# Optimization experiments

Hardware: AMD Instinct MI355X
Metric: run time of the kernel (lower is better)

The kernel has to match this reference:

```python
import jax, jax.numpy as jnp
import numpy as np

B, S, IN_DIM, HID, OUT_DIM, H = 2, 2048, 1024, 1024, 1024, 16
DH_IN = IN_DIM // H   # 64
DH_HID = HID // H     # 64


def setup_inputs() -> dict:
    key = jax.random.key(0)
    ks = jax.random.split(key, 12)
    sc_in = 1.0 / np.sqrt(DH_IN)
    sc_hid = 1.0 / np.sqrt(HID)
    return {
        "q": jax.random.normal(ks[0], (B, S, IN_DIM), jnp.float32),
        "k": jax.random.normal(ks[1], (B, S, IN_DIM), jnp.float32),
        "v": jax.random.normal(ks[2], (B, S, IN_DIM), jnp.float32),
        "mask": jax.random.randint(ks[3], (B, 1, S, S), 0, 2, jnp.int32),
        "Wq": jax.random.uniform(ks[4], (DH_HID, DH_IN), jnp.float32, -sc_in, sc_in),
        "bq": jax.random.uniform(ks[5], (DH_HID,), jnp.float32, -sc_in, sc_in),
        "Wk": jax.random.uniform(ks[6], (DH_HID, DH_IN), jnp.float32, -sc_in, sc_in),
        "bk": jax.random.uniform(ks[7], (DH_HID,), jnp.float32, -sc_in, sc_in),
        "Wv": jax.random.uniform(ks[8], (DH_HID, DH_IN), jnp.float32, -sc_in, sc_in),
        "bv": jax.random.uniform(ks[9], (DH_HID,), jnp.float32, -sc_in, sc_in),
        "Wo": jax.random.uniform(ks[10], (OUT_DIM, HID), jnp.float32, -sc_hid, sc_hid),
        "bo": jax.random.uniform(ks[11], (OUT_DIM,), jnp.float32, -sc_hid, sc_hid),
    }


def reference(q, k, v, mask, Wq, bq, Wk, bk, Wv, bv, Wo, bo):
    # Faithful to original: raw reshape head split (view), NOT a transpose split.
    q_i = q.reshape(B, H, S, DH_IN) @ Wq.T + bq   # [B,H,S,DH_HID]
    k_i = k.reshape(B, H, S, DH_IN) @ Wk.T + bk
    v_i = v.reshape(B, H, S, DH_IN) @ Wv.T + bv
    scores = jnp.einsum('bhqd,bhkd->bhqk', q_i, k_i) / jnp.sqrt(jnp.float32(DH_HID))
    scores = jnp.where(mask != 0, jnp.float32(-10000.0), scores)
    wv = jnp.einsum('bhqk,bhkd->bhqd', jax.nn.softmax(scores, axis=-1), v_i)
    # Faithful to original: raw reshape merge [B,H,S,dh] -> [B,S,H*dh].
    wv = wv.reshape(B, S, H * DH_HID)
    return wv @ Wo.T + bo
```

## Files before the change

### kernel.cpp

```cpp
#include <hip/hip_runtime.h>
#include <hip/hip_bf16.h>
#include <hip/hip_fp16.h>

#define NB 2
#define NS 2048
#define NHD 16
#define DH 64
#define NHID 1024
#define SD (NS*DH)
#define BHN (NB*NHD)

typedef _Float16 F16;
typedef _Float16 f16x8 __attribute__((ext_vector_type(8)));
typedef _Float16 f16x2 __attribute__((ext_vector_type(2)));
typedef float    f32x4  __attribute__((ext_vector_type(4)));
typedef float    f32x16 __attribute__((ext_vector_type(16)));
typedef unsigned short U16;
typedef unsigned long long U64;
typedef unsigned short u16x8 __attribute__((ext_vector_type(8)));

__device__ __forceinline__ f32x4 mfma16(f16x8 a, f16x8 b, f32x4 c) {
  return __builtin_amdgcn_mfma_f32_16x16x32_f16(a, b, c, 0, 0, 0);
}
__device__ __forceinline__ f32x16 mfma32(f16x8 a, f16x8 b, f32x16 c) {
  return __builtin_amdgcn_mfma_f32_32x32x16_f16(a, b, c, 0, 0, 0);
}
__device__ __forceinline__ unsigned pk2(float a, float b) {
  return __builtin_bit_cast(unsigned, __builtin_amdgcn_cvt_pkrtz(a, b));
}

__global__ __launch_bounds__(256) void k_prep(const int* __restrict__ mask,
                                              const float* __restrict__ Wo,
                                              U64* __restrict__ mb,
                                              F16* __restrict__ wob) {
  const int tid  = threadIdx.x;
  const int lane = tid & 63;
  const int wid  = blockIdx.x * 4 + (tid >> 6);
  const int nwords = NB * NS * (NS / 64);
  for (int w = wid; w < nwords; w += 4096) {
    int m = mask[(size_t)w * 64 + lane];
    U64 bits = __ballot(m != 0);
    if (lane == 0) mb[w] = bits;
  }
  int t = blockIdx.x * 256 + tid;
  float4 f = *(const float4*)(Wo + (size_t)t * 4);
  union { U16 u[4]; F16 h[4]; } o;
  o.h[0] = (F16)f.x; o.h[1] = (F16)f.y; o.h[2] = (F16)f.z; o.h[3] = (F16)f.w;
  *(ushort4*)(wob + (size_t)t * 4) = *(ushort4*)o.u;
}

__global__ __launch_bounds__(256) void k_proj(const float* __restrict__ qin,
    const float* __restrict__ kin, const float* __restrict__ vin,
    const float* __restrict__ Wq, const float* __restrict__ bq,
    const float* __restrict__ Wk, const float* __restrict__ bk,
    const float* __restrict__ Wv, const float* __restrict__ bv,
    F16* __restrict__ qh, F16* __restrict__ kh, F16* __restrict__ vt) {
  __shared__ float Xs[64][68];
  __shared__ F16   Ws[64][72];
  __shared__ float bs[64];
  __shared__ F16   Ts[64][72];

  const int tid = threadIdx.x;
  const int bh = blockIdx.x >> 5;
  const int rt = blockIdx.x & 31;
  const int b = bh >> 4, h = bh & 15;
  const int r0 = rt * 64;
  const size_t xbase = (size_t)b * NS * NHID + (size_t)h * SD + (size_t)r0 * DH;
  const int w = tid >> 6, lane = tid & 63, lm = lane & 15, lg = lane >> 4;
  (void)h;

  for (int t = 0; t < 3; ++t) {
    const float* Xin = (t == 0) ? qin : (t == 1) ? kin : vin;
    const float* Wt  = (t == 0) ? Wq  : (t == 1) ? Wk  : Wv;
    const float* bt  = (t == 0) ? bq  : (t == 1) ? bk  : bv;
    const float scale = (t == 0) ? 0.18033688f : 1.0f;
    __syncthreads();
#pragma unroll
    for (int it = 0; it < 4; ++it) {
      int f = it * 1024 + tid * 4;
      int r = f >> 6, c = f & 63;
      float4 xv = *(const float4*)(Xin + xbase + f);
      *(float4*)&Xs[r][c] = xv;
      float4 wv4 = *(const float4*)(Wt + f);
      union { U16 u[4]; F16 h4[4]; } wo;
      wo.h4[0] = (F16)(wv4.x * scale); wo.h4[1] = (F16)(wv4.y * scale);
      wo.h4[2] = (F16)(wv4.z * scale); wo.h4[3] = (F16)(wv4.w * scale);
      *(ushort4*)&Ws[r][c] = *(ushort4*)wo.u;
    }
    if (tid < 64) bs[tid] = bt[tid] * scale;
    __syncthreads();

    f16x8 af[2];
#pragma unroll
    for (int kk = 0; kk < 2; ++kk) {
      const float* sp = &Xs[w * 16 + lm][kk * 32 + lg * 8];
      union { F16 h8[8]; f16x8 v; } pk;
#pragma unroll
      for (int j = 0; j < 8; ++j) pk.h8[j] = (F16)sp[j];
      af[kk] = pk.v;
    }
    f32x4 acc[4];
#pragma unroll
    for (int nt = 0; nt < 4; ++nt) acc[nt] = (f32x4){0.f, 0.f, 0.f, 0.f};
#pragma unroll
    for (int kk = 0; kk < 2; ++kk) {
#pragma unroll
      for (int nt = 0; nt < 4; ++nt) {
        f16x8 bw = *(const f16x8*)&Ws[nt * 16 + lm][kk * 32 + lg * 8];
        acc[nt] = mfma16(af[kk], bw, acc[nt]);
      }
    }
    if (t < 2) {
      F16* dst = (t == 0) ? qh : kh;
#pragma unroll
      for (int nt = 0; nt < 4; ++nt)
#pragma unroll
        for (int rg = 0; rg < 4; ++rg) {
          int row = w * 16 + lg * 4 + rg;
          int col = nt * 16 + lm;
          dst[(size_t)bh * SD + (size_t)(r0 + row) * DH + col] =
              (F16)(acc[nt][rg] + bs[col]);
        }
    } else {
#pragma unroll
      for (int nt = 0; nt < 4; ++nt)
#pragma unroll
        for (int rg = 0; rg < 4; ++rg) {
          int row = w * 16 + lg * 4 + rg;
          int col = nt * 16 + lm;
          Ts[row][col] = (F16)(acc[nt][rg] + bs[col]);
        }
      __syncthreads();
      int d = tid >> 2, qq = tid & 3;
      size_t dst = (size_t)bh * SD + (size_t)d * NS + r0 + qq * 16;
#pragma unroll
      for (int half = 0; half < 2; ++half) {
        union { F16 h8[8]; u16x8 v; } pk;
#pragma unroll
        for (int i = 0; i < 8; ++i) {
          int r = (i < 4) ? (half * 4 + i) : (i + 4 + half * 4);
          pk.h8[i] = Ts[qq * 16 + r][d];
        }
        *(u16x8*)(vt + dst + half * 8) = pk.v;
      }
    }
  }
}

__global__ __launch_bounds__(256) void k_attn(const F16* __restrict__ qh,
    const F16* __restrict__ kh, const F16* __restrict__ vt,
    const U64* __restrict__ mb, F16* __restrict__ wvb) {
  __shared__ float bl[4][32];
  const int tid = threadIdx.x;
  const int w = tid >> 6, l = tid & 63;
  const int lq = l & 31, hi = l >> 5;
  const int tile = blockIdx.x * 4 + w;
  const int bh = tile >> 6;
  const int qt = tile & 63;
  const int b = bh >> 4;
  const int q0 = qt * 32;
  const size_t hb = (size_t)bh * SD;

  f16x8 qf[4];
#pragma unroll
  for (int kt = 0; kt < 4; ++kt)
    qf[kt] = *(const f16x8*)(qh + hb + (size_t)(q0 + lq) * DH + kt * 16 + hi * 8);

  f32x16 accO0, accO1;
#pragma unroll
  for (int r = 0; r < 16; ++r) { accO0[r] = 0.f; accO1[r] = 0.f; }
  float m_run = -1e30f, l_run = 0.f;

  const U64* mrow = mb + ((size_t)b * NS + q0 + lq) * (NS / 64);
  const F16* kb = kh + hb;
  const F16* vb = vt + hb;
  const f16x2 one2 = {(F16)1.f, (F16)1.f};

  for (int c64 = 0; c64 < 32; ++c64) {
    const int kv0 = c64 * 64;
    U64 wm = mrow[c64];
    f32x16 s0, s1;
#pragma unroll
    for (int r = 0; r < 16; ++r) { s0[r] = 0.f; s1[r] = 0.f; }
#pragma unroll
    for (int kt = 0; kt < 4; ++kt) {
      f16x8 kf0 = *(const f16x8*)(kb + (size_t)(kv0 + lq) * DH + kt * 16 + hi * 8);
      f16x8 kf1 = *(const f16x8*)(kb + (size_t)(kv0 + 32 + lq) * DH + kt * 16 + hi * 8);
      s0 = mfma32(kf0, qf[kt], s0);
      s1 = mfma32(kf1, qf[kt], s1);
    }
    float cmax = fmaxf(s0[0], s1[0]);
#pragma unroll
    for (int r = 1; r < 16; ++r) cmax = fmaxf(cmax, fmaxf(s0[r], s1[r]));
    cmax = fmaxf(cmax, __shfl_xor(cmax, 32, 64));
    if (__any(cmax > m_run + 8.0f)) {
      float nm = fmaxf(m_run, cmax);
      float al = __builtin_amdgcn_exp2f(m_run - nm);
      m_run = nm;
      l_run *= al;
      bl[w][lq] = al;
      asm volatile("s_waitcnt lgkmcnt(0)" ::: "memory");
      __builtin_amdgcn_sched_barrier(0);
      float4 g0 = *(const float4*)&bl[w][hi * 4];
      float4 g1 = *(const float4*)&bl[w][8 + hi * 4];
      float4 g2 = *(const float4*)&bl[w][16 + hi * 4];
      float4 g3 = *(const float4*)&bl[w][24 + hi * 4];
      float av[16] = {g0.x,g0.y,g0.z,g0.w, g1.x,g1.y,g1.z,g1.w,
                      g2.x,g2.y,g2.z,g2.w, g3.x,g3.y,g3.z,g3.w};
#pragma unroll
      for (int r = 0; r < 16; ++r) { accO0[r] *= av[r]; accO1[r] *= av[r]; }
    }
#pragma unroll
    for (int r = 0; r < 16; ++r) {
      s0[r] = __builtin_amdgcn_exp2f(s0[r] - m_run);
      s1[r] = __builtin_amdgcn_exp2f(s1[r] - m_run);
    }
    unsigned u0 = ((unsigned)wm) >> (hi * 4);
    unsigned u1 = ((unsigned)(wm >> 32)) >> (hi * 4);
#pragma unroll
    for (int r = 0; r < 16; ++r) {
      const int sh = (r & 3) + 8 * (r >> 2);
      s0[r] = ((u0 >> sh) & 1u) ? 0.f : s0[r];
      s1[r] = ((u1 >> sh) & 1u) ? 0.f : s1[r];
    }
#pragma unroll
    for (int c = 0; c < 4; ++c) {
      const int rb = (c & 1) * 8;
      unsigned w0, w1, w2, w3;
      if (c < 2) {
        w0 = pk2(s0[rb + 0], s0[rb + 1]);
        w1 = pk2(s0[rb + 2], s0[rb + 3]);
        w2 = pk2(s0[rb + 4], s0[rb + 5]);
        w3 = pk2(s0[rb + 6], s0[rb + 7]);
      } else {
        w0 = pk2(s1[rb + 0], s1[rb + 1]);
        w1 = pk2(s1[rb + 2], s1[rb + 3]);
        w2 = pk2(s1[rb + 4], s1[rb + 5]);
        w3 = pk2(s1[rb + 6], s1[rb + 7]);
      }
      union { unsigned u[4]; f16x8 v; } P;
      P.u[0] = w0; P.u[1] = w1; P.u[2] = w2; P.u[3] = w3;
      l_run = __builtin_amdgcn_fdot2(__builtin_bit_cast(f16x2, w0), one2, l_run, false);
      l_run = __builtin_amdgcn_fdot2(__builtin_bit_cast(f16x2, w1), one2, l_run, false);
      l_run = __builtin_amdgcn_fdot2(__builtin_bit_cast(f16x2, w2), one2, l_run, false);
      l_run = __builtin_amdgcn_fdot2(__builtin_bit_cast(f16x2, w3), one2, l_run, false);
      f16x8 v0 = *(const f16x8*)(vb + (size_t)lq * NS + kv0 + c * 16 + hi * 8);
      f16x8 v1 = *(const f16x8*)(vb + (size_t)(32 + lq) * NS + kv0 + c * 16 + hi * 8);
      accO0 = mfma32(P.v, v0, accO0);
      accO1 = mfma32(P.v, v1, accO1);
    }
  }
  l_run += __shfl_xor(l_run, 32, 64);
  float inv = 1.0f / l_run;
  bl[w][lq] = inv;
  asm volatile("s_waitcnt lgkmcnt(0)" ::: "memory");
  __builtin_amdgcn_sched_barrier(0);
  float4 g0 = *(const float4*)&bl[w][hi * 4];
  float4 g1 = *(const float4*)&bl[w][8 + hi * 4];
  float4 g2 = *(const float4*)&bl[w][16 + hi * 4];
  float4 g3 = *(const float4*)&bl[w][24 + hi * 4];
  float iv[16] = {g0.x,g0.y,g0.z,g0.w, g1.x,g1.y,g1.z,g1.w,
                  g2.x,g2.y,g2.z,g2.w, g3.x,g3.y,g3.z,g3.w};
#pragma unroll
  for (int r = 0; r < 16; ++r) {
    const int row = q0 + (r & 3) + 8 * (r >> 2) + 4 * hi;
    wvb[hb + (size_t)row * DH + lq]      = (F16)(accO0[r] * iv[r]);
    wvb[hb + (size_t)row * DH + 32 + lq] = (F16)(accO1[r] * iv[r]);
  }
}

__global__ __launch_bounds__(256) void k_oproj(const F16* __restrict__ A,
    const F16* __restrict__ Bw, const float* __restrict__ bo,
    float* __restrict__ out) {
  __shared__ F16 As[64][72];
  __shared__ F16 Bs[64][72];
  const int tid = threadIdx.x;
  const int tc0 = blockIdx.x * 64;
  const int tr0 = blockIdx.y * 64;
  const int w = tid >> 6, lane = tid & 63, lm = lane & 15, lg = lane >> 4;
  f32x4 acc[4];
#pragma unroll
  for (int j = 0; j < 4; ++j) acc[j] = (f32x4){0.f, 0.f, 0.f, 0.f};

  for (int kt = 0; kt < 16; ++kt) {
    const int k0 = kt * 64;
    __syncthreads();
#pragma unroll
    for (int it = 0; it < 2; ++it) {
      int c = it * 256 + tid;
      int r = c >> 3, c8 = c & 7;
      *(u16x8*)&As[r][c8 * 8] =
          *(const u16x8*)(A + (size_t)(tr0 + r) * NHID + k0 + c8 * 8);
      *(u16x8*)&Bs[r][c8 * 8] =
          *(const u16x8*)(Bw + (size_t)(tc0 + r) * NHID + k0 + c8 * 8);
    }
    __syncthreads();
#pragma unroll
    for (int kk = 0; kk < 2; ++kk) {
      f16x8 af = *(const f16x8*)&As[w * 16 + lm][kk * 32 + lg * 8];
#pragma unroll
      for (int nt = 0; nt < 4; ++nt) {
        f16x8 bfr = *(const f16x8*)&Bs[nt * 16 + lm][kk * 32 + lg * 8];
        acc[nt] = mfma16(af, bfr, acc[nt]);
      }
    }
  }
#pragma unroll
  for (int nt = 0; nt < 4; ++nt) {
    float bias = bo[tc0 + nt * 16 + lm];
#pragma unroll
    for (int rg = 0; rg < 4; ++rg) {
      int row = tr0 + w * 16 + lg * 4 + rg;
      int col = tc0 + nt * 16 + lm;
      out[(size_t)row * NHID + col] = acc[nt][rg] + bias;
    }
  }
}

extern "C" void kernel_launch(void* const* d_in, const int* in_sizes, int n_in,
                              void* d_out, int out_size, void* d_ws, size_t ws_size,
                              hipStream_t stream) {
  const float* q  = (const float*)d_in[0];
  const float* k  = (const float*)d_in[1];
  const float* v  = (const float*)d_in[2];
  const int*  mask = (const int*)d_in[3];
  const float* Wq = (const float*)d_in[4];
  const float* bq = (const float*)d_in[5];
  const float* Wk = (const float*)d_in[6];
  const float* bk = (const float*)d_in[7];
  const float* Wv = (const float*)d_in[8];
  const float* bv = (const float*)d_in[9];
  const float* Wo = (const float*)d_in[10];
  const float* bo = (const float*)d_in[11];
  float* out = (float*)d_out;
  char* ws = (char*)d_ws;

  F16* qh  = (F16*)(ws);
  F16* kh  = (F16*)(ws + ((size_t)8  << 20));
  F16* vt  = (F16*)(ws + ((size_t)16 << 20));
  F16* wvb = (F16*)(ws + ((size_t)24 << 20));
  U64* mb  = (U64*)(ws + ((size_t)32 << 20));
  F16* wob = (F16*)(ws + ((size_t)33 << 20));

  hipLaunchKernelGGL(k_prep, dim3(1024), dim3(256), 0, stream, mask, Wo, mb, wob);
  hipLaunchKernelGGL(k_proj, dim3(1024), dim3(256), 0, stream,
                     q, k, v, Wq, bq, Wk, bk, Wv, bv, qh, kh, vt);
  hipLaunchKernelGGL(k_attn, dim3(512), dim3(256), 0, stream, qh, kh, vt, mb, wvb);
  hipLaunchKernelGGL(k_oproj, dim3(16, 64), dim3(256), 0, stream, wvb, wob, bo, out);
}
```

Baseline: 293.5 us.

## Split attention KV range across wave pairs and enlarge output-projection tiles

Each attention query tile is now processed by two waves, each covering half of the key/value range. The two partial softmax states (max, sum, output) are merged through shared memory, and the grid doubles to 1024 blocks for more parallelism and latency hiding. The mask word is prefetched one iteration ahead, and the row max now uses a tree reduction. The output projection moves from 64x64 to 128x128 tiles with a 4x4 MFMA block per wave for better data reuse, at the cost of more registers and fewer blocks.

```diff
diff --git a/kernel.cpp b/kernel.cpp
--- a/kernel.cpp
+++ b/kernel.cpp
@@ -147,14 +147,19 @@
   }
 }
 
-__global__ __launch_bounds__(256) void k_attn(const F16* __restrict__ qh,
+__global__ __launch_bounds__(256, 4) void k_attn(const F16* __restrict__ qh,
     const F16* __restrict__ kh, const F16* __restrict__ vt,
     const U64* __restrict__ mb, F16* __restrict__ wvb) {
   __shared__ float bl[4][32];
+  __shared__ float ms[2][2][32];
+  __shared__ float ls[2][2][32];
+  __shared__ float Os[2][32][64];
   const int tid = threadIdx.x;
   const int w = tid >> 6, l = tid & 63;
   const int lq = l & 31, hi = l >> 5;
-  const int tile = blockIdx.x * 4 + w;
+  const int pair = w >> 1;
+  const int half = w & 1;
+  const int tile = blockIdx.x * 2 + pair;
   const int bh = tile >> 6;
   const int qt = tile & 63;
   const int b = bh >> 4;
@@ -176,9 +181,12 @@
   const F16* vb = vt + hb;
   const f16x2 one2 = {(F16)1.f, (F16)1.f};
 
-  for (int c64 = 0; c64 < 32; ++c64) {
+  const int cbeg = half * 16, cend = cbeg + 16;
+  U64 wm = mrow[cbeg];
+  for (int c64 = cbeg; c64 < cend; ++c64) {
     const int kv0 = c64 * 64;
-    U64 wm = mrow[c64];
+    U64 wm_cur = wm;
+    if (c64 + 1 < cend) wm = mrow[c64 + 1];
     f32x16 s0, s1;
 #pragma unroll
     for (int r = 0; r < 16; ++r) { s0[r] = 0.f; s1[r] = 0.f; }
@@ -189,9 +197,13 @@
       s0 = mfma32(kf0, qf[kt], s0);
       s1 = mfma32(kf1, qf[kt], s1);
     }
-    float cmax = fmaxf(s0[0], s1[0]);
-#pragma unroll
-    for (int r = 1; r < 16; ++r) cmax = fmaxf(cmax, fmaxf(s0[r], s1[r]));
+    float tm[8];
+#pragma unroll
+    for (int i = 0; i < 8; ++i)
+      tm[i] = fmaxf(fmaxf(s0[i], s0[i + 8]), fmaxf(s1[i], s1[i + 8]));
+#pragma unroll
+    for (int i = 0; i < 4; ++i) tm[i] = fmaxf(tm[i], tm[i + 4]);
+    float cmax = fmaxf(fmaxf(tm[0], tm[1]), fmaxf(tm[2], tm[3]));
     cmax = fmaxf(cmax, __shfl_xor(cmax, 32, 64));
     if (__any(cmax > m_run + 8.0f)) {
       float nm = fmaxf(m_run, cmax);
@@ -215,8 +227,8 @@
       s0[r] = __builtin_amdgcn_exp2f(s0[r] - m_run);
       s1[r] = __builtin_amdgcn_exp2f(s1[r] - m_run);
     }
-    unsigned u0 = ((unsigned)wm) >> (hi * 4);
-    unsigned u1 = ((unsigned)(wm >> 32)) >> (hi * 4);
+    unsigned u0 = ((unsigned)wm_cur) >> (hi * 4);
+    unsigned u1 = ((unsigned)(wm_cur >> 32)) >> (hi * 4);
 #pragma unroll
     for (int r = 0; r < 16; ++r) {
       const int sh = (r & 3) + 8 * (r >> 2);
@@ -251,69 +263,107 @@
     }
   }
   l_run += __shfl_xor(l_run, 32, 64);
-  float inv = 1.0f / l_run;
-  bl[w][lq] = inv;
-  asm volatile("s_waitcnt lgkmcnt(0)" ::: "memory");
-  __builtin_amdgcn_sched_barrier(0);
-  float4 g0 = *(const float4*)&bl[w][hi * 4];
-  float4 g1 = *(const float4*)&bl[w][8 + hi * 4];
-  float4 g2 = *(const float4*)&bl[w][16 + hi * 4];
-  float4 g3 = *(const float4*)&bl[w][24 + hi * 4];
-  float iv[16] = {g0.x,g0.y,g0.z,g0.w, g1.x,g1.y,g1.z,g1.w,
-                  g2.x,g2.y,g2.z,g2.w, g3.x,g3.y,g3.z,g3.w};
-#pragma unroll
-  for (int r = 0; r < 16; ++r) {
-    const int row = q0 + (r & 3) + 8 * (r >> 2) + 4 * hi;
-    wvb[hb + (size_t)row * DH + lq]      = (F16)(accO0[r] * iv[r]);
-    wvb[hb + (size_t)row * DH + 32 + lq] = (F16)(accO1[r] * iv[r]);
+  ms[pair][half][lq] = m_run;
+  ls[pair][half][lq] = l_run;
+  __syncthreads();
+  float av[16], iv[16];
+#pragma unroll
+  for (int g = 0; g < 4; ++g) {
+    float4 M0 = *(const float4*)&ms[pair][0][g * 8 + hi * 4];
+    float4 M1 = *(const float4*)&ms[pair][1][g * 8 + hi * 4];
+    float4 L0 = *(const float4*)&ls[pair][0][g * 8 + hi * 4];
+    float4 L1 = *(const float4*)&ls[pair][1][g * 8 + hi * 4];
+    const float m0a[4] = {M0.x, M0.y, M0.z, M0.w};
+    const float m1a[4] = {M1.x, M1.y, M1.z, M1.w};
+    const float l0a[4] = {L0.x, L0.y, L0.z, L0.w};
+    const float l1a[4] = {L1.x, L1.y, L1.z, L1.w};
+#pragma unroll
+    for (int j = 0; j < 4; ++j) {
+      const int r = g * 4 + j;
+      float mn = fmaxf(m0a[j], m1a[j]);
+      float A0 = __builtin_amdgcn_exp2f(m0a[j] - mn);
+      float A1 = __builtin_amdgcn_exp2f(m1a[j] - mn);
+      av[r] = half ? A1 : A0;
+      iv[r] = 1.0f / (l0a[j] * A0 + l1a[j] * A1);
+    }
+  }
+  if (half == 0) {
+#pragma unroll
+    for (int r = 0; r < 16; ++r) {
+      const int row = (r & 3) + 8 * (r >> 2) + 4 * hi;
+      Os[pair][row][lq]      = accO0[r] * av[r];
+      Os[pair][row][32 + lq] = accO1[r] * av[r];
+    }
+  }
+  __syncthreads();
+  if (half == 1) {
+#pragma unroll
+    for (int r = 0; r < 16; ++r) {
+      const int row = (r & 3) + 8 * (r >> 2) + 4 * hi;
+      float o0 = (Os[pair][row][lq]      + accO0[r] * av[r]) * iv[r];
+      float o1 = (Os[pair][row][32 + lq] + accO1[r] * av[r]) * iv[r];
+      wvb[hb + (size_t)(q0 + row) * DH + lq]      = (F16)o0;
+      wvb[hb + (size_t)(q0 + row) * DH + 32 + lq] = (F16)o1;
+    }
   }
 }
 
 __global__ __launch_bounds__(256) void k_oproj(const F16* __restrict__ A,
     const F16* __restrict__ Bw, const float* __restrict__ bo,
     float* __restrict__ out) {
-  __shared__ F16 As[64][72];
-  __shared__ F16 Bs[64][72];
+  __shared__ F16 Ab[128][72];
+  __shared__ F16 Bb[128][72];
   const int tid = threadIdx.x;
-  const int tc0 = blockIdx.x * 64;
-  const int tr0 = blockIdx.y * 64;
+  const int tr0 = blockIdx.y * 128;
+  const int tc0 = blockIdx.x * 128;
   const int w = tid >> 6, lane = tid & 63, lm = lane & 15, lg = lane >> 4;
-  f32x4 acc[4];
-#pragma unroll
-  for (int j = 0; j < 4; ++j) acc[j] = (f32x4){0.f, 0.f, 0.f, 0.f};
+  const int wr = (w >> 1) * 64, wc = (w & 1) * 64;
+  f32x4 acc[4][4];
+#pragma unroll
+  for (int i = 0; i < 4; ++i)
+#pragma unroll
+    for (int j = 0; j < 4; ++j) acc[i][j] = (f32x4){0.f, 0.f, 0.f, 0.f};
 
   for (int kt = 0; kt < 16; ++kt) {
     const int k0 = kt * 64;
     __syncthreads();
 #pragma unroll
-    for (int it = 0; it < 2; ++it) {
+    for (int it = 0; it < 4; ++it) {
       int c = it * 256 + tid;
       int r = c >> 3, c8 = c & 7;
-      *(u16x8*)&As[r][c8 * 8] =
+      *(u16x8*)&Ab[r][c8 * 8] =
           *(const u16x8*)(A + (size_t)(tr0 + r) * NHID + k0 + c8 * 8);
-      *(u16x8*)&Bs[r][c8 * 8] =
+      *(u16x8*)&Bb[r][c8 * 8] =
           *(const u16x8*)(Bw + (size_t)(tc0 + r) * NHID + k0 + c8 * 8);
     }
     __syncthreads();
 #pragma unroll
     for (int kk = 0; kk < 2; ++kk) {
-      f16x8 af = *(const f16x8*)&As[w * 16 + lm][kk * 32 + lg * 8];
-#pragma unroll
-      for (int nt = 0; nt < 4; ++nt) {
-        f16x8 bfr = *(const f16x8*)&Bs[nt * 16 + lm][kk * 32 + lg * 8];
-        acc[nt] = mfma16(af, bfr, acc[nt]);
+      f16x8 af[4], bfr[4];
+#pragma unroll
+      for (int mt = 0; mt < 4; ++mt)
+        af[mt] = *(const f16x8*)&Ab[wr + mt * 16 + lm][kk * 32 + lg * 8];
+#pragma unroll
+      for (int nt = 0; nt < 4; ++nt)
+        bfr[nt] = *(const f16x8*)&Bb[wc + nt * 16 + lm][kk * 32 + lg * 8];
+#pragma unroll
+      for (int mt = 0; mt < 4; ++mt)
+#pragma unroll
+        for (int nt = 0; nt < 4; ++nt)
+          acc[mt][nt] = mfma16(af[mt], bfr[nt], acc[mt][nt]);
+    }
+  }
+#pragma unroll
+  for (int nt = 0; nt < 4; ++nt) {
+    float bias = bo[tc0 + wc + nt * 16 + lm];
+#pragma unroll
+    for (int mt = 0; mt < 4; ++mt)
+#pragma unroll
+      for (int rg = 0; rg < 4; ++rg) {
+        int row = tr0 + wr + mt * 16 + lg * 4 + rg;
+        int col = tc0 + wc + nt * 16 + lm;
+        out[(size_t)row * NHID + col] = acc[mt][nt][rg] + bias;
       }
-    }
-  }
-#pragma unroll
-  for (int nt = 0; nt < 4; ++nt) {
-    float bias = bo[tc0 + nt * 16 + lm];
-#pragma unroll
-    for (int rg = 0; rg < 4; ++rg) {
-      int row = tr0 + w * 16 + lg * 4 + rg;
-      int col = tc0 + nt * 16 + lm;
-      out[(size_t)row * NHID + col] = acc[nt][rg] + bias;
-    }
   }
 }
 
@@ -345,6 +395,6 @@
   hipLaunchKernelGGL(k_prep, dim3(1024), dim3(256), 0, stream, mask, Wo, mb, wob);
   hipLaunchKernelGGL(k_proj, dim3(1024), dim3(256), 0, stream,
                      q, k, v, Wq, bq, Wk, bk, Wv, bv, qh, kh, vt);
-  hipLaunchKernelGGL(k_attn, dim3(512), dim3(256), 0, stream, qh, kh, vt, mb, wvb);
-  hipLaunchKernelGGL(k_oproj, dim3(16, 64), dim3(256), 0, stream, wvb, wob, bo, out);
-}
+  hipLaunchKernelGGL(k_attn, dim3(1024), dim3(256), 0, stream, qh, kh, vt, mb, wvb);
+  hipLaunchKernelGGL(k_oproj, dim3(8, 32), dim3(256), 0, stream, wvb, wob, bo, out);
+}
```

Result: slower. 303.5 us (+3.4%).
